# Optimization experiments

Hardware: AMD Instinct MI355X
Metric: run time of the kernel (lower is better)

The kernel has to match this reference:

```python
import jax, jax.numpy as jnp
import numpy as np

N_ITERS = 2
N_NODES = 50000
N_EDGES = 400000
NODE_DIM = 128
EDGE_DIM = 128
MLP_HIDDEN = 128


def _gru_cell(x, h, W_ih, W_hh, b_ih, b_hh):
    # torch.nn.GRUCell math. W_ih: [3H, in], W_hh: [3H, H]
    gi = x @ W_ih.T + b_ih
    gh = h @ W_hh.T + b_hh
    i_r, i_z, i_n = jnp.split(gi, 3, axis=-1)
    h_r, h_z, h_n = jnp.split(gh, 3, axis=-1)
    r = jax.nn.sigmoid(i_r + h_r)
    z = jax.nn.sigmoid(i_z + h_z)
    n = jnp.tanh(i_n + r * h_n)
    return (1.0 - z) * n + z * h


def _edge_softmax(logits, dst, num_nodes):
    # logits: [E], normalized over incoming edges of each dst node
    m = jax.ops.segment_max(logits, dst, num_segments=num_nodes)
    e = jnp.exp(logits - m[dst])
    s = jax.ops.segment_sum(e, dst, num_segments=num_nodes)
    return e / s[dst]


def setup_inputs() -> dict:
    key = jax.random.key(0)
    ks = jax.random.split(key, 20)
    s = 0.05
    inp = {
        'nf': jax.random.normal(ks[0], (N_NODES, NODE_DIM), jnp.float32),
        'ef': jax.random.normal(ks[1], (N_EDGES, EDGE_DIM), jnp.float32),
        'src': jax.random.randint(ks[2], (N_EDGES,), 0, N_NODES, jnp.int32),
        'dst': jax.random.randint(ks[3], (N_EDGES,), 0, N_NODES, jnp.int32),
        # edge GRUCell: input 2*node_dim -> hidden edge_dim
        'eW_ih': s * jax.random.normal(ks[4], (3 * EDGE_DIM, 2 * NODE_DIM), jnp.float32),
        'eW_hh': s * jax.random.normal(ks[5], (3 * EDGE_DIM, EDGE_DIM), jnp.float32),
        'eb_ih': s * jax.random.normal(ks[6], (3 * EDGE_DIM,), jnp.float32),
        'eb_hh': s * jax.random.normal(ks[7], (3 * EDGE_DIM,), jnp.float32),
        # node GRUCell: input edge_dim -> hidden node_dim
        'nW_ih': s * jax.random.normal(ks[8], (3 * NODE_DIM, EDGE_DIM), jnp.float32),
        'nW_hh': s * jax.random.normal(ks[9], (3 * NODE_DIM, NODE_DIM), jnp.float32),
        'nb_ih': s * jax.random.normal(ks[10], (3 * NODE_DIM,), jnp.float32),
        'nb_hh': s * jax.random.normal(ks[11], (3 * NODE_DIM,), jnp.float32),
        # attention MLP: edge_dim -> hidden -> 1
        'aW1': s * jax.random.normal(ks[12], (EDGE_DIM, MLP_HIDDEN), jnp.float32),
        'ab1': jnp.zeros((MLP_HIDDEN,), jnp.float32),
        'aW2': s * jax.random.normal(ks[13], (MLP_HIDDEN, 1), jnp.float32),
        'ab2': jnp.zeros((1,), jnp.float32),
    }
    return inp


def reference(nf, ef, src, dst, eW_ih, eW_hh, eb_ih, eb_hh,
              nW_ih, nW_hh, nb_ih, nb_hh, aW1, ab1, aW2, ab2):
    num_nodes = nf.shape[0]
    for _ in range(N_ITERS):
        # per-edge GRU update: input = [src_h ; dst_h], hidden = edge feature
        x_e = jnp.concatenate([nf[src], nf[dst]], axis=-1)  # [E, 2*node_dim]
        uef = _gru_cell(x_e, ef, eW_ih, eW_hh, eb_ih, eb_hh)  # [E, edge_dim]
        # attention MLP + edge softmax over destination neighborhoods
        logits = (jax.nn.relu(uef @ aW1 + ab1) @ aW2 + ab2)[:, 0]  # [E]
        attn = _edge_softmax(logits, dst, num_nodes)  # [E]
        # weighted scatter-sum aggregation to destination nodes
        agg_m = jax.ops.segment_sum(uef * attn[:, None], dst, num_segments=num_nodes)
        # node GRU update
        unf = _gru_cell(agg_m, nf, nW_ih, nW_hh, nb_ih, nb_hh)  # [N, node_dim]
        nf, ef = unf, uef
    return (nf, ef)
```

## Files before the change

kernel.cpp:

```cpp
#include <hip/hip_runtime.h>

#define NN 50000
#define NE 400000
#define DIM 128

typedef __bf16 bf16x8 __attribute__((ext_vector_type(8)));
typedef float f32x4 __attribute__((ext_vector_type(4)));
typedef unsigned short u16;

#define MFMA16 __builtin_amdgcn_mfma_f32_16x16x32_bf16

__device__ __forceinline__ u16 f2b(float f){ __bf16 b=(__bf16)f; return __builtin_bit_cast(u16,b); }
__device__ __forceinline__ float b2f(u16 h){ unsigned u = ((unsigned)h)<<16; return __builtin_bit_cast(float,u); }
__device__ __forceinline__ float sigm(float x){ return 1.0f/(1.0f+__expf(-x)); }
__device__ __forceinline__ float tanh_(float x){ float e=__expf(2.0f*x); return 1.0f-2.0f/(e+1.0f); }
__device__ __forceinline__ bf16x8 ldb8(const u16* p){ return *reinterpret_cast<const bf16x8*>(p); }

#define GLOAD_LDS(gp, lp) __builtin_amdgcn_global_load_lds( \
    (const __attribute__((address_space(1))) void*)(gp),    \
    (__attribute__((address_space(3))) void*)(lp), 16, 0, 0)

__global__ void f2b_kernel(const float* __restrict__ in, u16* __restrict__ out, int n4){
  int i = blockIdx.x*blockDim.x + threadIdx.x;
  int st = gridDim.x*blockDim.x;
  for (; i<n4; i+=st){
    float4 v = reinterpret_cast<const float4*>(in)[i];
    ushort4 o = { f2b(v.x), f2b(v.y), f2b(v.z), f2b(v.w) };
    reinterpret_cast<ushort4*>(out)[i] = o;
  }
}

__global__ void transpose128_kernel(const float* __restrict__ in, u16* __restrict__ out){
  int i = blockIdx.x*blockDim.x + threadIdx.x;
  int k = i>>7, n = i&127;
  out[n*128+k] = f2b(in[i]);
}

__global__ void zero_kernel(int* p, int n){
  int i = blockIdx.x*blockDim.x + threadIdx.x; if (i<n) p[i]=0;
}
__global__ void hist_kernel(const int* __restrict__ dst, int* __restrict__ counts, int n){
  int i = blockIdx.x*blockDim.x + threadIdx.x; if (i<n) atomicAdd(&counts[dst[i]],1);
}
__global__ void scan_kernel(const int* __restrict__ counts, int* __restrict__ rowp,
                            int* __restrict__ cursor, int n){
  __shared__ int buf[1024];
  __shared__ int run;
  const int t = threadIdx.x;
  if (t==0) run = 0;
  __syncthreads();
  for (int base=0; base<n; base+=1024){
    int v = (base+t<n) ? counts[base+t] : 0;
    buf[t]=v; __syncthreads();
    for (int off=1; off<1024; off<<=1){
      int x = (t>=off) ? buf[t-off] : 0;
      __syncthreads();
      buf[t]+=x; __syncthreads();
    }
    int incl = buf[t];
    int br = run;
    __syncthreads();
    if (base+t<n){ int ex = br+incl-v; rowp[base+t]=ex; cursor[base+t]=ex; }
    if (t==1023) run = br+incl;
    __syncthreads();
  }
  if (t==0) rowp[n]=run;
}
__global__ void scatter_kernel(const int* __restrict__ dst, int* __restrict__ cursor,
                               int* __restrict__ eids, int n){
  int i = blockIdx.x*blockDim.x + threadIdx.x;
  if (i<n){ int p = atomicAdd(&cursor[dst[i]],1); eids[p]=i; }
}

__global__ __launch_bounds__(512, 4)
void edge_kernel(const int* __restrict__ src, const int* __restrict__ dst,
                 const u16* __restrict__ nfb, u16* __restrict__ efb,
                 const u16* __restrict__ Wih, const u16* __restrict__ Whh,
                 const float* __restrict__ bih, const float* __restrict__ bhh,
                 const u16* __restrict__ aW1T, const float* __restrict__ ab1,
                 const float* __restrict__ aW2, const float* __restrict__ ab2,
                 float* __restrict__ logits, float* __restrict__ ef32out)
{
  __shared__ __align__(16) u16 wbuf[36*512];
  __shared__ __align__(16) u16 etile[8*16*128];
  const int wave = threadIdx.x>>6, lane = threadIdx.x&63;
  const int r16 = lane&15, kq = lane>>4;
  const long base = (long)blockIdx.x*128 + wave*16;
  const long e = base + r16;
  char* tb = (char*)(etile + wave*16*DIM);

  auto stage = [&](int c){
    if (c < 8){
      for (int f = wave; f < 36; f += 8){
        const u16* g;
        if (f < 24){ const int gt = f>>3, s = f&7;
          g = Wih + (long)(gt*128 + c*16 + r16)*256 + s*32 + kq*8; }
        else { const int q = f-24, gt = q>>2, s = q&3;
          g = Whh + (long)(gt*128 + c*16 + r16)*128 + s*32 + kq*8; }
        GLOAD_LDS(g, wbuf + f*512);
      }
    } else {
      for (int f = wave; f < 32; f += 8){
        const int t = f>>2, s = f&3;
        GLOAD_LDS(aW1T + (long)(t*16 + r16)*128 + s*32 + kq*8, wbuf + f*512);
      }
    }
  };

  const u16* sp = nfb + (long)src[e]*DIM;
  const u16* dp = nfb + (long)dst[e]*DIM;
  const u16* ep = efb + e*DIM;
  bf16x8 ag[8], ae[4];
#pragma unroll
  for (int s=0;s<4;++s){
    ag[s]   = ldb8(sp + s*32 + kq*8);
    ag[s+4] = ldb8(dp + s*32 + kq*8);
    ae[s]   = ldb8(ep + s*32 + kq*8);
  }
#pragma unroll
  for (int s=0;s<4;++s)
    *(uint4*)(tb + r16*256 + ((s*64 + kq*16) ^ ((r16&7)<<4))) = __builtin_bit_cast(uint4, ae[s]);
  stage(0);
  __syncthreads();

  const f32x4 vzero = {0.f,0.f,0.f,0.f};
  const u16* lbase = wbuf + lane*8;

#pragma unroll 1
  for (int c=0;c<8;++c){
    const int oc = c*16 + r16;
    const float bir=bih[oc], biz=bih[DIM+oc], bin=bih[2*DIM+oc];
    const float bhr=bhh[oc], bhz=bhh[DIM+oc], bhn=bhh[2*DIM+oc];

    f32x4 ar=vzero, az=vzero, an=vzero, hr=vzero, hz=vzero, hn=vzero;
#pragma unroll
    for (int s=0;s<8;++s){
      ar = MFMA16(ag[s], ldb8(lbase + ( s   )*512), ar,0,0,0);
      az = MFMA16(ag[s], ldb8(lbase + ( 8+s )*512), az,0,0,0);
      an = MFMA16(ag[s], ldb8(lbase + (16+s )*512), an,0,0,0);
    }
#pragma unroll
    for (int s=0;s<4;++s){
      hr = MFMA16(ae[s], ldb8(lbase + (24+s)*512), hr,0,0,0);
      hz = MFMA16(ae[s], ldb8(lbase + (28+s)*512), hz,0,0,0);
      hn = MFMA16(ae[s], ldb8(lbase + (32+s)*512), hn,0,0,0);
    }
    __syncthreads();
    stage(c+1);
#pragma unroll
    for (int r=0;r<4;++r){
      const int row = kq*4+r;
      char* slot = tb + row*256 + ((oc*2 - c*32 + c*32) ^ 0);
      (void)slot;
      const int boff = row*256 + (((c*32) + r16*2) ^ ((row&7)<<4));
      float h0 = b2f(*(const u16*)(tb + boff));
      float rg = sigm(ar[r]+bir + hr[r]+bhr);
      float zg = sigm(az[r]+biz + hz[r]+bhz);
      float ng = tanh_(an[r]+bin + rg*(hn[r]+bhn));
      float u  = (1.0f-zg)*ng + zg*h0;
      *(u16*)(tb + boff) = f2b(u);
      if (ef32out) ef32out[(base+row)*DIM+oc] = u;
    }
    __syncthreads();
  }

  bf16x8 ua[4];
#pragma unroll
  for (int s=0;s<4;++s)
    ua[s] = __builtin_bit_cast(bf16x8, *(const uint4*)(tb + r16*256 + ((s*64 + kq*16) ^ ((r16&7)<<4))));
  float part[4] = {0.f,0.f,0.f,0.f};
#pragma unroll 1
  for (int t=0;t<8;++t){
    f32x4 h = vzero;
#pragma unroll
    for (int s=0;s<4;++s)
      h = MFMA16(ua[s], ldb8(lbase + (t*4+s)*512), h,0,0,0);
    const int cc = t*16 + r16;
    const float b1 = ab1[cc], w2 = aW2[cc];
#pragma unroll
    for (int r=0;r<4;++r) part[r] += fmaxf(h[r]+b1, 0.f)*w2;
  }
#pragma unroll
  for (int off=1; off<16; off<<=1){
#pragma unroll
    for (int r=0;r<4;++r) part[r] += __shfl_xor(part[r], off, 64);
  }
  if (r16==0){
    const float b2v = ab2[0];
#pragma unroll
    for (int r=0;r<4;++r) logits[base + kq*4 + r] = part[r] + b2v;
  }

#pragma unroll
  for (int i2=0;i2<4;++i2){
    const int idx = i2*64 + lane;
    const int row = idx>>4, slot = idx&15;
    uint4 val = *(const uint4*)(tb + row*256 + ((slot*16) ^ ((row&7)<<4)));
    *(uint4*)(efb + (base+row)*DIM + slot*8) = val;
  }
}

__global__ __launch_bounds__(256)
void agg_kernel(const int* __restrict__ rowp, const int* __restrict__ eids,
                const float* __restrict__ logits, const u16* __restrict__ uefb,
                u16* __restrict__ aggb)
{
  const int wave = threadIdx.x>>6, lane = threadIdx.x&63;
  const int v = blockIdx.x*4 + wave;
  if (v>=NN) return;
  const int p0 = rowp[v], deg = rowp[v+1]-p0;
  float ax=0.f, ay=0.f;
  if (deg>0){
    float mx = -__builtin_inff();
    for (int i=lane; i<deg; i+=64) mx = fmaxf(mx, logits[eids[p0+i]]);
#pragma unroll
    for (int off=32; off; off>>=1) mx = fmaxf(mx, __shfl_xor(mx, off, 64));
    float ss = 0.f;
    for (int i=lane; i<deg; i+=64) ss += __expf(logits[eids[p0+i]] - mx);
#pragma unroll
    for (int off=32; off; off>>=1) ss += __shfl_xor(ss, off, 64);
    const float inv = 1.0f/ss;
    int i = 0;
    for (; i+2<=deg; i+=2){
      const int e0 = eids[p0+i], e1 = eids[p0+i+1];
      const float l0 = logits[e0], l1 = logits[e1];
      const unsigned q0 = *reinterpret_cast<const unsigned*>(uefb + (long)e0*DIM + lane*2);
      const unsigned q1 = *reinterpret_cast<const unsigned*>(uefb + (long)e1*DIM + lane*2);
      const float a0 = __expf(l0-mx)*inv, a1 = __expf(l1-mx)*inv;
      ax += a0*b2f((u16)q0) + a1*b2f((u16)q1);
      ay += a0*b2f((u16)(q0>>16)) + a1*b2f((u16)(q1>>16));
    }
    if (i<deg){
      const int e0 = eids[p0+i];
      const float a0 = __expf(logits[e0]-mx)*inv;
      const unsigned q0 = *reinterpret_cast<const unsigned*>(uefb + (long)e0*DIM + lane*2);
      ax += a0*b2f((u16)q0);
      ay += a0*b2f((u16)(q0>>16));
    }
  }
  unsigned pack = (unsigned)f2b(ax) | ((unsigned)f2b(ay)<<16);
  *reinterpret_cast<unsigned*>(aggb + (long)v*DIM + lane*2) = pack;
}

__global__ __launch_bounds__(512, 4)
void node_kernel(const u16* __restrict__ aggb, u16* __restrict__ nfb,
                 const float* nf32, float* unf32,
                 const u16* __restrict__ Wih, const u16* __restrict__ Whh,
                 const float* __restrict__ bih, const float* __restrict__ bhh)
{
  __shared__ __align__(16) u16 wbuf[24*512];
  const int wave = threadIdx.x>>6, lane = threadIdx.x&63;
  const int r16 = lane&15, kq = lane>>4;
  const long tbase = (long)blockIdx.x*128 + wave*16;
  const long v = tbase + r16;
  const long vcl = (v < NN) ? v : (NN-1);

  auto stage = [&](int c){
    if (c >= 8) return;
    for (int f = wave; f < 24; f += 8){
      const u16* g;
      if (f < 12){ const int gt = f>>2, s = f&3;
        g = Wih + (long)(gt*128 + c*16 + r16)*128 + s*32 + kq*8; }
      else { const int q = f-12, gt = q>>2, s = q&3;
        g = Whh + (long)(gt*128 + c*16 + r16)*128 + s*32 + kq*8; }
      GLOAD_LDS(g, wbuf + f*512);
    }
  };

  bf16x8 xa[4], ha[4];
#pragma unroll
  for (int s=0;s<4;++s){
    xa[s] = ldb8(aggb + vcl*DIM + s*32 + kq*8);
    ha[s] = ldb8(nfb  + vcl*DIM + s*32 + kq*8);
  }
  stage(0);
  __syncthreads();

  const f32x4 vzero = {0.f,0.f,0.f,0.f};
  const u16* lbase = wbuf + lane*8;

#pragma unroll 1
  for (int c=0;c<8;++c){
    const int oc = c*16 + r16;
    const float bir=bih[oc], biz=bih[DIM+oc], bin=bih[2*DIM+oc];
    const float bhr=bhh[oc], bhz=bhh[DIM+oc], bhn=bhh[2*DIM+oc];
    float h0p[4];
#pragma unroll
    for (int r=0;r<4;++r){
      const long rr = tbase + kq*4 + r;
      h0p[r] = (rr < NN) ? nf32[rr*DIM+oc] : 0.f;
    }
    f32x4 ar=vzero, az=vzero, an=vzero, hr=vzero, hz=vzero, hn=vzero;
#pragma unroll
    for (int s=0;s<4;++s){
      ar=MFMA16(xa[s], ldb8(lbase + ( s   )*512), ar,0,0,0);
      az=MFMA16(xa[s], ldb8(lbase + ( 4+s)*512), az,0,0,0);
      an=MFMA16(xa[s], ldb8(lbase + ( 8+s)*512), an,0,0,0);
      hr=MFMA16(ha[s], ldb8(lbase + (12+s)*512), hr,0,0,0);
      hz=MFMA16(ha[s], ldb8(lbase + (16+s)*512), hz,0,0,0);
      hn=MFMA16(ha[s], ldb8(lbase + (20+s)*512), hn,0,0,0);
    }
    __syncthreads();
    stage(c+1);
#pragma unroll
    for (int r=0;r<4;++r){
      const long rr = tbase + kq*4 + r;
      if (rr < NN){
        float rg = sigm(ar[r]+bir + hr[r]+bhr);
        float zg = sigm(az[r]+biz + hz[r]+bhz);
        float ng = tanh_(an[r]+bin + rg*(hn[r]+bhn));
        float u  = (1.0f-zg)*ng + zg*h0p[r];
        unf32[rr*DIM+oc] = u;
        nfb[rr*DIM+oc] = f2b(u);
      }
    }
    __syncthreads();
  }
}

extern "C" void kernel_launch(void* const* d_in, const int* in_sizes, int n_in,
                              void* d_out, int out_size, void* d_ws, size_t ws_size,
                              hipStream_t stream)
{
  const float* nf_in = (const float*)d_in[0];
  const float* ef_in = (const float*)d_in[1];
  const int*   src   = (const int*)d_in[2];
  const int*   dst   = (const int*)d_in[3];
  const float* eWih  = (const float*)d_in[4];
  const float* eWhh  = (const float*)d_in[5];
  const float* ebih  = (const float*)d_in[6];
  const float* ebhh  = (const float*)d_in[7];
  const float* nWih  = (const float*)d_in[8];
  const float* nWhh  = (const float*)d_in[9];
  const float* nbih  = (const float*)d_in[10];
  const float* nbhh  = (const float*)d_in[11];
  const float* aW1   = (const float*)d_in[12];
  const float* ab1   = (const float*)d_in[13];
  const float* aW2   = (const float*)d_in[14];
  const float* ab2   = (const float*)d_in[15];

  float* nf_out = (float*)d_out;
  float* ef_out = nf_out + (size_t)NN*DIM;

  char* p = (char*)d_ws;
  auto carve = [&](size_t bytes)->void*{ void* r = (void*)p; p += (bytes + 255) & ~(size_t)255; return r; };
  u16* efb    = (u16*)carve((size_t)NE*DIM*2);
  u16* nfb    = (u16*)carve((size_t)NN*DIM*2);
  u16* aggb   = (u16*)carve((size_t)NN*DIM*2);
  float* logits = (float*)carve((size_t)NE*4);
  int* eids   = (int*)carve((size_t)NE*4);
  int* counts = (int*)carve((size_t)NN*4);
  int* rowp   = (int*)carve((size_t)(NN+1)*4);
  int* cursor = (int*)carve((size_t)NN*4);
  u16* bWih   = (u16*)carve((size_t)384*256*2);
  u16* bWhh   = (u16*)carve((size_t)384*128*2);
  u16* bnWih  = (u16*)carve((size_t)384*128*2);
  u16* bnWhh  = (u16*)carve((size_t)384*128*2);
  u16* baW1T  = (u16*)carve((size_t)128*128*2);

  f2b_kernel<<<2048,256,0,stream>>>(nf_in, nfb, NN*DIM/4);
  f2b_kernel<<<2048,256,0,stream>>>(ef_in, efb, NE*DIM/4);
  f2b_kernel<<<96,256,0,stream>>>(eWih, bWih, 384*256/4);
  f2b_kernel<<<48,256,0,stream>>>(eWhh, bWhh, 384*128/4);
  f2b_kernel<<<48,256,0,stream>>>(nWih, bnWih, 384*128/4);
  f2b_kernel<<<48,256,0,stream>>>(nWhh, bnWhh, 384*128/4);
  transpose128_kernel<<<64,256,0,stream>>>(aW1, baW1T);

  zero_kernel<<<(NN+255)/256,256,0,stream>>>(counts, NN);
  hist_kernel<<<(NE+255)/256,256,0,stream>>>(dst, counts, NE);
  scan_kernel<<<1,1024,0,stream>>>(counts, rowp, cursor, NN);
  scatter_kernel<<<(NE+255)/256,256,0,stream>>>(dst, cursor, eids, NE);

  for (int it=0; it<2; ++it){
    const float* nf_cur = (it==0) ? nf_in : nf_out;
    float* efout32 = (it==1) ? ef_out : nullptr;
    edge_kernel<<<NE/128,512,0,stream>>>(src, dst, nfb, efb,
                                         bWih, bWhh, ebih, ebhh,
                                         baW1T, ab1, aW2, ab2, logits, efout32);
    agg_kernel<<<(NN+3)/4,256,0,stream>>>(rowp, eids, logits, efb, aggb);
    node_kernel<<<(NN+127)/128,512,0,stream>>>(aggb, nfb, nf_cur, nf_out,
                                               bnWih, bnWhh, nbih, nbhh);
  }
}
```

Before: 903.9 us.

## Double-buffer GRU weight staging in LDS and drop the edge feature tile

Both the edge and node GRU kernels now keep two LDS weight buffers. The load for the next output chunk is issued at the start of each iteration, so weight fetches overlap the MFMA work instead of waiting behind a barrier. The edge kernel no longer stages edge features in a swizzled LDS tile. It reads the old hidden values straight from global memory, writes bf16 results back element by element, and reloads them from global for the attention MLP. That frees the LDS the larger weight buffers need, but it adds uncoalesced 2-byte global stores and a reliance on global write visibility within the block.

```diff
diff --git a/kernel.cpp b/kernel.cpp
--- a/kernel.cpp
+++ b/kernel.cpp
@@ -81,15 +81,14 @@
                  const float* __restrict__ aW2, const float* __restrict__ ab2,
                  float* __restrict__ logits, float* __restrict__ ef32out)
 {
-  __shared__ __align__(16) u16 wbuf[36*512];
-  __shared__ __align__(16) u16 etile[8*16*128];
+  __shared__ __align__(16) u16 wbuf[2*36*512];
   const int wave = threadIdx.x>>6, lane = threadIdx.x&63;
   const int r16 = lane&15, kq = lane>>4;
   const long base = (long)blockIdx.x*128 + wave*16;
   const long e = base + r16;
-  char* tb = (char*)(etile + wave*16*DIM);
 
   auto stage = [&](int c){
+    u16* bufp = wbuf + (c&1)*36*512;
     if (c < 8){
       for (int f = wave; f < 36; f += 8){
         const u16* g;
@@ -97,12 +96,12 @@
           g = Wih + (long)(gt*128 + c*16 + r16)*256 + s*32 + kq*8; }
         else { const int q = f-24, gt = q>>2, s = q&3;
           g = Whh + (long)(gt*128 + c*16 + r16)*128 + s*32 + kq*8; }
-        GLOAD_LDS(g, wbuf + f*512);
+        GLOAD_LDS(g, bufp + f*512);
       }
-    } else {
+    } else if (c == 8){
       for (int f = wave; f < 32; f += 8){
         const int t = f>>2, s = f&3;
-        GLOAD_LDS(aW1T + (long)(t*16 + r16)*128 + s*32 + kq*8, wbuf + f*512);
+        GLOAD_LDS(aW1T + (long)(t*16 + r16)*128 + s*32 + kq*8, bufp + f*512);
       }
     }
   };
@@ -117,64 +116,59 @@
     ag[s+4] = ldb8(dp + s*32 + kq*8);
     ae[s]   = ldb8(ep + s*32 + kq*8);
   }
-#pragma unroll
-  for (int s=0;s<4;++s)
-    *(uint4*)(tb + r16*256 + ((s*64 + kq*16) ^ ((r16&7)<<4))) = __builtin_bit_cast(uint4, ae[s]);
   stage(0);
   __syncthreads();
 
   const f32x4 vzero = {0.f,0.f,0.f,0.f};
-  const u16* lbase = wbuf + lane*8;
 
 #pragma unroll 1
   for (int c=0;c<8;++c){
+    stage(c+1);
     const int oc = c*16 + r16;
     const float bir=bih[oc], biz=bih[DIM+oc], bin=bih[2*DIM+oc];
     const float bhr=bhh[oc], bhz=bhh[DIM+oc], bhn=bhh[2*DIM+oc];
-
+    float h0p[4];
+#pragma unroll
+    for (int r=0;r<4;++r) h0p[r] = b2f(efb[(base+kq*4+r)*DIM + oc]);
+
+    const u16* lb = wbuf + (c&1)*36*512 + lane*8;
     f32x4 ar=vzero, az=vzero, an=vzero, hr=vzero, hz=vzero, hn=vzero;
 #pragma unroll
     for (int s=0;s<8;++s){
-      ar = MFMA16(ag[s], ldb8(lbase + ( s   )*512), ar,0,0,0);
-      az = MFMA16(ag[s], ldb8(lbase + ( 8+s )*512), az,0,0,0);
-      an = MFMA16(ag[s], ldb8(lbase + (16+s )*512), an,0,0,0);
+      ar = MFMA16(ag[s], ldb8(lb + ( s   )*512), ar,0,0,0);
+      az = MFMA16(ag[s], ldb8(lb + ( 8+s )*512), az,0,0,0);
+      an = MFMA16(ag[s], ldb8(lb + (16+s )*512), an,0,0,0);
     }
 #pragma unroll
     for (int s=0;s<4;++s){
-      hr = MFMA16(ae[s], ldb8(lbase + (24+s)*512), hr,0,0,0);
-      hz = MFMA16(ae[s], ldb8(lbase + (28+s)*512), hz,0,0,0);
-      hn = MFMA16(ae[s], ldb8(lbase + (32+s)*512), hn,0,0,0);
-    }
-    __syncthreads();
-    stage(c+1);
+      hr = MFMA16(ae[s], ldb8(lb + (24+s)*512), hr,0,0,0);
+      hz = MFMA16(ae[s], ldb8(lb + (28+s)*512), hz,0,0,0);
+      hn = MFMA16(ae[s], ldb8(lb + (32+s)*512), hn,0,0,0);
+    }
 #pragma unroll
     for (int r=0;r<4;++r){
-      const int row = kq*4+r;
-      char* slot = tb + row*256 + ((oc*2 - c*32 + c*32) ^ 0);
-      (void)slot;
-      const int boff = row*256 + (((c*32) + r16*2) ^ ((row&7)<<4));
-      float h0 = b2f(*(const u16*)(tb + boff));
+      const long er = base + kq*4 + r;
       float rg = sigm(ar[r]+bir + hr[r]+bhr);
       float zg = sigm(az[r]+biz + hz[r]+bhz);
       float ng = tanh_(an[r]+bin + rg*(hn[r]+bhn));
-      float u  = (1.0f-zg)*ng + zg*h0;
-      *(u16*)(tb + boff) = f2b(u);
-      if (ef32out) ef32out[(base+row)*DIM+oc] = u;
+      float u  = (1.0f-zg)*ng + zg*h0p[r];
+      efb[er*DIM+oc] = f2b(u);
+      if (ef32out) ef32out[er*DIM+oc] = u;
     }
     __syncthreads();
   }
 
   bf16x8 ua[4];
 #pragma unroll
-  for (int s=0;s<4;++s)
-    ua[s] = __builtin_bit_cast(bf16x8, *(const uint4*)(tb + r16*256 + ((s*64 + kq*16) ^ ((r16&7)<<4))));
+  for (int s=0;s<4;++s) ua[s] = ldb8(ep + s*32 + kq*8);
+  const u16* lb = wbuf + lane*8;
   float part[4] = {0.f,0.f,0.f,0.f};
 #pragma unroll 1
   for (int t=0;t<8;++t){
     f32x4 h = vzero;
 #pragma unroll
     for (int s=0;s<4;++s)
-      h = MFMA16(ua[s], ldb8(lbase + (t*4+s)*512), h,0,0,0);
+      h = MFMA16(ua[s], ldb8(lb + (t*4+s)*512), h,0,0,0);
     const int cc = t*16 + r16;
     const float b1 = ab1[cc], w2 = aW2[cc];
 #pragma unroll
@@ -189,14 +183,6 @@
     const float b2v = ab2[0];
 #pragma unroll
     for (int r=0;r<4;++r) logits[base + kq*4 + r] = part[r] + b2v;
-  }
-
-#pragma unroll
-  for (int i2=0;i2<4;++i2){
-    const int idx = i2*64 + lane;
-    const int row = idx>>4, slot = idx&15;
-    uint4 val = *(const uint4*)(tb + row*256 + ((slot*16) ^ ((row&7)<<4)));
-    *(uint4*)(efb + (base+row)*DIM + slot*8) = val;
   }
 }
 
@@ -248,7 +234,7 @@
                  const u16* __restrict__ Wih, const u16* __restrict__ Whh,
                  const float* __restrict__ bih, const float* __restrict__ bhh)
 {
-  __shared__ __align__(16) u16 wbuf[24*512];
+  __shared__ __align__(16) u16 wbuf[2*24*512];
   const int wave = threadIdx.x>>6, lane = threadIdx.x&63;
   const int r16 = lane&15, kq = lane>>4;
   const long tbase = (long)blockIdx.x*128 + wave*16;
@@ -257,13 +243,14 @@
 
   auto stage = [&](int c){
     if (c >= 8) return;
+    u16* bufp = wbuf + (c&1)*24*512;
     for (int f = wave; f < 24; f += 8){
       const u16* g;
       if (f < 12){ const int gt = f>>2, s = f&3;
         g = Wih + (long)(gt*128 + c*16 + r16)*128 + s*32 + kq*8; }
       else { const int q = f-12, gt = q>>2, s = q&3;
         g = Whh + (long)(gt*128 + c*16 + r16)*128 + s*32 + kq*8; }
-      GLOAD_LDS(g, wbuf + f*512);
+      GLOAD_LDS(g, bufp + f*512);
     }
   };
 
@@ -277,10 +264,10 @@
   __syncthreads();
 
   const f32x4 vzero = {0.f,0.f,0.f,0.f};
-  const u16* lbase = wbuf + lane*8;
 
 #pragma unroll 1
   for (int c=0;c<8;++c){
+    stage(c+1);
     const int oc = c*16 + r16;
     const float bir=bih[oc], biz=bih[DIM+oc], bin=bih[2*DIM+oc];
     const float bhr=bhh[oc], bhz=bhh[DIM+oc], bhn=bhh[2*DIM+oc];
@@ -290,18 +277,17 @@
       const long rr = tbase + kq*4 + r;
       h0p[r] = (rr < NN) ? nf32[rr*DIM+oc] : 0.f;
     }
+    const u16* lb = wbuf + (c&1)*24*512 + lane*8;
     f32x4 ar=vzero, az=vzero, an=vzero, hr=vzero, hz=vzero, hn=vzero;
 #pragma unroll
     for (int s=0;s<4;++s){
-      ar=MFMA16(xa[s], ldb8(lbase + ( s   )*512), ar,0,0,0);
-      az=MFMA16(xa[s], ldb8(lbase + ( 4+s)*512), az,0,0,0);
-      an=MFMA16(xa[s], ldb8(lbase + ( 8+s)*512), an,0,0,0);
-      hr=MFMA16(ha[s], ldb8(lbase + (12+s)*512), hr,0,0,0);
-      hz=MFMA16(ha[s], ldb8(lbase + (16+s)*512), hz,0,0,0);
-      hn=MFMA16(ha[s], ldb8(lbase + (20+s)*512), hn,0,0,0);
-    }
-    __syncthreads();
-    stage(c+1);
+      ar=MFMA16(xa[s], ldb8(lb + ( s   )*512), ar,0,0,0);
+      az=MFMA16(xa[s], ldb8(lb + ( 4+s)*512), az,0,0,0);
+      an=MFMA16(xa[s], ldb8(lb + ( 8+s)*512), an,0,0,0);
+      hr=MFMA16(ha[s], ldb8(lb + (12+s)*512), hr,0,0,0);
+      hz=MFMA16(ha[s], ldb8(lb + (16+s)*512), hz,0,0,0);
+      hn=MFMA16(ha[s], ldb8(lb + (20+s)*512), hn,0,0,0);
+    }
 #pragma unroll
     for (int r=0;r<4;++r){
       const long rr = tbase + kq*4 + r;
```

New measurement: 928.9 us. 1.03x slower.
